# Kernel tuning notes

Hardware: AMD Instinct MI355X
Metric: run time of the kernel (lower is better)

Reference implementation:

```python
import jax, jax.numpy as jnp
import numpy as np

H = 512   # hidden_size
E = 512   # choice embedding dim (== hidden in the dummy init)
B = 256   # batch
T = 64    # arg sequence length
V = 10000 # number of choices


def setup_inputs() -> dict:
    key = jax.random.key(0)
    ks = jax.random.split(key, 10)
    s = 0.05
    return {
        "init_state": jax.random.normal(ks[0], (B, H), jnp.float32),
        "choice_embed": jax.random.normal(ks[1], (V, E), jnp.float32),
        "arg_seq": jax.random.randint(ks[2], (B, T), 0, V, jnp.int64),
        # flax LSTMCell equivalent: fused gate weights (order i, f, g, o)
        "Wx": jax.random.normal(ks[3], (E, 4 * H), jnp.float32) * s,
        "Wh": jax.random.normal(ks[4], (H, 4 * H), jnp.float32) * s,
        "b": jnp.zeros((4 * H,), jnp.float32),
        # MLP step-score head: concat(H, E) -> 256 -> 1
        "W1": jax.random.normal(ks[5], (H + E, 256), jnp.float32) * s,
        "b1": jnp.zeros((256,), jnp.float32),
        "W2": jax.random.normal(ks[6], (256, 1), jnp.float32) * s,
        "b2": jnp.zeros((1,), jnp.float32),
    }


def _forward(init_state, choice_embed, arg_seq, Wx, Wh, b, W1, b1, W2, b2):
    # initial carry: zeros + init_state, for both c and h
    c0 = init_state
    h0 = init_state
    x_seq = choice_embed[arg_seq]            # [B, T, E] embedding gather
    xs = jnp.swapaxes(x_seq, 0, 1)           # [T, B, E] for scan

    def step(carry, x):
        c, h = carry
        gates = x @ Wx + h @ Wh + b          # [B, 4H]
        i, f, g, o = jnp.split(gates, 4, axis=-1)
        i = jax.nn.sigmoid(i)
        f = jax.nn.sigmoid(f)
        g = jnp.tanh(g)
        o = jax.nn.sigmoid(o)
        c2 = f * c + i * g
        h2 = o * jnp.tanh(c2)
        return (c2, h2), h2

    _, hs = jax.lax.scan(step, (c0, h0), xs)  # hs: [T, B, H]
    hs = jnp.swapaxes(hs, 0, 1)               # [B, T, H]
    # state fed to the score head at step t is the hidden BEFORE consuming x_t
    state = jnp.concatenate((h0[:, None, :], hs[:, :-1, :]), axis=1)  # [B, T, H]
    state = state.reshape(-1, H)               # [B*T, H]

    feat = jnp.concatenate((state, x_seq.reshape(-1, E)), axis=-1)    # [B*T, H+E]
    hid = jax.nn.relu(feat @ W1 + b1)
    score = hid @ W2 + b2                      # [B*T, 1]
    step_scores = score.reshape(-1, T)         # [B, T]
    return jnp.sum(step_scores, axis=-1, keepdims=True)  # [B, 1]


def reference(init_state, choice_embed, arg_seq, Wx, Wh, b, W1, b1, W2, b2):
    return _forward(init_state, choice_embed, arg_seq, Wx, Wh, b, W1, b1, W2, b2)
```

## Files before the change

### kernel.cpp

```cpp
#include <hip/hip_runtime.h>
#include <hip/hip_bf16.h>
#include <math.h>

#define H   512
#define E   512
#define B_  256
#define T_  64
#define G4  2048
#define C1  256
#define BT  16384

#define SPIN_CAP (1 << 22)

typedef __attribute__((ext_vector_type(8))) short  short8;
typedef __attribute__((ext_vector_type(4))) float  f32x4;
typedef __attribute__((ext_vector_type(4))) int    i32x4;
typedef __attribute__((ext_vector_type(4))) unsigned short ushort4v;
typedef unsigned short ushort;
typedef unsigned long long u64;

#define PITCH_US 520

#define BAR_LGKM() asm volatile("s_waitcnt lgkmcnt(0)\n\ts_barrier" ::: "memory")
#define BAR_ALL()  asm volatile("s_waitcnt vmcnt(0) lgkmcnt(0)\n\ts_barrier" ::: "memory")

__device__ __forceinline__ ushort f2bf(float x) {
    unsigned u = __builtin_bit_cast(unsigned, x);
    unsigned r = (u + 0x7FFFu + ((u >> 16) & 1u)) >> 16;
    return (ushort)r;
}
__device__ __forceinline__ float fast_sig(float x) {
    return __builtin_amdgcn_rcpf(1.f + __expf(-x));
}
__device__ __forceinline__ float fast_tanh(float x) {
    return 1.f - 2.f * __builtin_amdgcn_rcpf(1.f + __expf(2.f * x));
}

#define LOAD4_SC0(v0,v1,v2,v3,p0,p1,p2,p3) \
  asm volatile("global_load_dwordx4 %0, %4, off sc0\n\t" \
               "global_load_dwordx4 %1, %5, off sc0\n\t" \
               "global_load_dwordx4 %2, %6, off sc0\n\t" \
               "global_load_dwordx4 %3, %7, off sc0\n\t" \
               "s_waitcnt vmcnt(0)" \
               : "=&v"(v0), "=&v"(v1), "=&v"(v2), "=&v"(v3) \
               : "v"(p0), "v"(p1), "v"(p2), "v"(p3) : "memory")
#define LOAD4_SC01(v0,v1,v2,v3,p0,p1,p2,p3) \
  asm volatile("global_load_dwordx4 %0, %4, off sc0 sc1\n\t" \
               "global_load_dwordx4 %1, %5, off sc0 sc1\n\t" \
               "global_load_dwordx4 %2, %6, off sc0 sc1\n\t" \
               "global_load_dwordx4 %3, %7, off sc0 sc1\n\t" \
               "s_waitcnt vmcnt(0)" \
               : "=&v"(v0), "=&v"(v1), "=&v"(v2), "=&v"(v3) \
               : "v"(p0), "v"(p1), "v"(p2), "v"(p3) : "memory")

__global__ __launch_bounds__(256) void prep_weights(
    const float* __restrict__ Wx, const float* __restrict__ Wh,
    const float* __restrict__ W1,
    ushort* __restrict__ WxT, ushort* __restrict__ WhT, ushort* __restrict__ W1T)
{
    __shared__ float t[32][33];
    int bx = blockIdx.x;
    const float* in; ushort* out; int K, N, k0, n0;
    if (bx < 1024)       { in = Wx; out = WxT; K = 512;  N = 2048; k0 = (bx >> 6) * 32; n0 = (bx & 63) * 32; }
    else if (bx < 2048)  { bx -= 1024; in = Wh; out = WhT; K = 512;  N = 2048; k0 = (bx >> 6) * 32; n0 = (bx & 63) * 32; }
    else                 { bx -= 2048; in = W1; out = W1T; K = 1024; N = 256;  k0 = (bx >> 3) * 32; n0 = (bx & 7) * 32; }
    const int tr = threadIdx.x >> 3;
    const int tc = (threadIdx.x & 7) * 4;
    float4 v = *(const float4*)(in + (size_t)(k0 + tr) * N + n0 + tc);
    t[tr][tc + 0] = v.x; t[tr][tc + 1] = v.y; t[tr][tc + 2] = v.z; t[tr][tc + 3] = v.w;
    __syncthreads();
    ushort4v o = { f2bf(t[tc + 0][tr]), f2bf(t[tc + 1][tr]),
                   f2bf(t[tc + 2][tr]), f2bf(t[tc + 3][tr]) };
    *(ushort4v*)(out + (size_t)(n0 + tr) * K + k0 + tc) = o;
}

__global__ __launch_bounds__(128) void gather_embed_bf16(
    const float* __restrict__ emb, const int* __restrict__ idx,
    ushort* __restrict__ X)
{
    const int r = blockIdx.x;
    const int v = idx[r];
    const int c = threadIdx.x * 4;
    float4 f = *(const float4*)(emb + (size_t)v * E + c);
    ushort4v o = { f2bf(f.x), f2bf(f.y), f2bf(f.z), f2bf(f.w) };
    *(ushort4v*)(X + (size_t)r * E + c) = o;
}

__global__ __launch_bounds__(128) void init_prep(
    const float* __restrict__ init, ushort* __restrict__ h0,
    ushort* __restrict__ S)
{
    const int r = blockIdx.x;
    const int c = threadIdx.x * 4;
    float4 f = *(const float4*)(init + (size_t)r * H + c);
    ushort4v o = { f2bf(f.x), f2bf(f.y), f2bf(f.z), f2bf(f.w) };
    *(ushort4v*)(h0 + (size_t)r * H + c) = o;
    *(ushort4v*)(S + ((size_t)r * T_) * H + c) = o;
}

__global__ __launch_bounds__(256) void zero_buf(int* p, int n) {
    int i = blockIdx.x * 256 + threadIdx.x;
    if (i < n) p[i] = 0;
}

__global__ __launch_bounds__(256, 1) void lstm_fused_main(
    const ushort* __restrict__ WhT, const ushort* __restrict__ WxT,
    const ushort* __restrict__ Xbf, const float* __restrict__ bg,
    const float*  __restrict__ init_state, const ushort* __restrict__ h0,
    ushort* __restrict__ pp0, ushort* __restrict__ pp1,
    ushort* __restrict__ S, int* __restrict__ xcd_tbl, int* __restrict__ cnts)
{
    __shared__ __align__(16) ushort hsh[16 * PITCH_US];
    __shared__ __align__(16) ushort xsh[2][16 * PITCH_US];
    __shared__ int exl[256];

    const int tid  = threadIdx.x;
    const int wave = tid >> 6, lane = tid & 63;
    const int quad = lane >> 4, l16 = lane & 15;

    int xcd;
    asm volatile("s_getreg_b32 %0, hwreg(HW_REG_XCC_ID)" : "=s"(xcd));
    if (tid == 0)
        __hip_atomic_store(&xcd_tbl[blockIdx.x], (xcd & 7) + 1,
                           __ATOMIC_RELAXED, __HIP_MEMORY_SCOPE_AGENT);
    if (wave == 0) {
        for (int it = 0; it < SPIN_CAP; ++it) {
            int miss = 0;
#pragma unroll
            for (int j = 0; j < 4; ++j) {
                int i = lane + j * 64;
                int v = __hip_atomic_load(&xcd_tbl[i], __ATOMIC_RELAXED,
                                          __HIP_MEMORY_SCOPE_AGENT);
                exl[i] = (v == 0) ? 0 : (v - 1);
                if (v == 0) miss = 1;
            }
            if (!__any(miss)) break;
            __builtin_amdgcn_s_sleep(4);
        }
    }
    BAR_LGKM();

    int g = 0, m = 0, loc = 0;
    {
        int cntx[8] = {0,0,0,0,0,0,0,0};
        for (int i = 0; i < 256; ++i) cntx[exl[i] & 7]++;
        int take[8], base[8], tA = 0;
        for (int x = 0; x < 8; ++x) {
            int tk = cntx[x] >> 4;
            if (tA + tk > 16) tk = 16 - tA;
            take[x] = tk; base[x] = tA; tA += tk;
        }
        int rc[8] = {0,0,0,0,0,0,0,0}, lc = 0;
        for (int i = 0; i < 256; ++i) {
            int x = exl[i] & 7, r = rc[x]++;
            if ((r >> 4) < take[x]) {
                if (i == (int)blockIdx.x) { g = base[x] + (r >> 4); m = r & 15; loc = 1; }
            } else {
                if (i == (int)blockIdx.x) { g = tA + (lc >> 4); m = lc & 15; loc = 0; }
                lc++;
            }
        }
    }

    const int n0   = g * 16;
    const int jw   = m * 32 + wave * 8;
    const int koff = quad * 8;
    const int ccol = jw + (quad & 1) * 4;
    const int myrow = n0 + l16;

    short8 af[2][16], ax[2][16];
#pragma unroll
    for (int mf = 0; mf < 2; ++mf) {
        const int gate = mf * 2 + (l16 >> 3);
        const size_t rowoff = (size_t)(gate * 512 + jw + (l16 & 7)) * 512 + koff;
        const ushort* bh = WhT + rowoff;
        const ushort* bx = WxT + rowoff;
#pragma unroll
        for (int kk = 0; kk < 16; ++kk) {
            af[mf][kk] = *(const short8*)(bh + kk * 32);
            ax[mf][kk] = *(const short8*)(bx + kk * 32);
        }
    }

    float bgi[4], bgf[4], bgg[4], bgo[4];
#pragma unroll
    for (int r = 0; r < 4; ++r) {
        bgi[r] = bg[ccol + r];
        bgf[r] = bg[512 + ccol + r];
        bgg[r] = bg[1024 + ccol + r];
        bgo[r] = bg[1536 + ccol + r];
    }

    float c[4];
    {
        const float* ip = init_state + (size_t)myrow * H + ccol;
#pragma unroll
        for (int r = 0; r < 4; ++r) c[r] = ip[r];
    }

    int gr[4], gc[4], lo[4];
#pragma unroll
    for (int j = 0; j < 4; ++j) {
        int lin = tid + j * 256;
        gr[j] = lin >> 6; gc[j] = lin & 63;
        lo[j] = gr[j] * PITCH_US + gc[j] * 8;
    }

#pragma unroll
    for (int j = 0; j < 4; ++j) {
        i32x4 v = *(const i32x4*)(Xbf + ((size_t)(n0 + gr[j]) * T_) * H + gc[j] * 8);
        *(i32x4*)&xsh[0][lo[j]] = v;
    }
    BAR_LGKM();

    int* cnt = cnts + g * 32;
    const int frag_base = l16 * PITCH_US + quad * 8;

    for (int t = 0; t < T_ - 1; ++t) {
        i32x4 xv0, xv1, xv2, xv3;
        const int have_x = (t + 1 < T_ - 1);
        if (have_x) {
            xv0 = *(const i32x4*)(Xbf + ((size_t)(n0 + gr[0]) * T_ + t + 1) * H + gc[0] * 8);
            xv1 = *(const i32x4*)(Xbf + ((size_t)(n0 + gr[1]) * T_ + t + 1) * H + gc[1] * 8);
            xv2 = *(const i32x4*)(Xbf + ((size_t)(n0 + gr[2]) * T_ + t + 1) * H + gc[2] * 8);
            xv3 = *(const i32x4*)(Xbf + ((size_t)(n0 + gr[3]) * T_ + t + 1) * H + gc[3] * 8);
        }

        f32x4 ax0 = {}, ax1 = {};
        {
            const ushort* xb = xsh[t & 1];
#pragma unroll
            for (int kk = 0; kk < 16; ++kk) {
                short8 b = *(const short8*)&xb[frag_base + kk * 32];
                ax0 = __builtin_amdgcn_mfma_f32_16x16x32_bf16(ax[0][kk], b, ax0, 0, 0, 0);
                ax1 = __builtin_amdgcn_mfma_f32_16x16x32_bf16(ax[1][kk], b, ax1, 0, 0, 0);
            }
        }

        if (t > 0) {
            const int tgt = t << 4;
            for (int it = 0; it < SPIN_CAP; ++it) {
                if (__hip_atomic_load(cnt, __ATOMIC_RELAXED,
                                      __HIP_MEMORY_SCOPE_AGENT) >= tgt) break;
                __builtin_amdgcn_s_sleep(1);
            }
        }

        {
            const ushort* hin = (t == 0) ? h0 : ((t & 1) ? pp0 : pp1);
            const ushort* p0 = hin + (size_t)(n0 + gr[0]) * H + gc[0] * 8;
            const ushort* p1 = hin + (size_t)(n0 + gr[1]) * H + gc[1] * 8;
            const ushort* p2 = hin + (size_t)(n0 + gr[2]) * H + gc[2] * 8;
            const ushort* p3 = hin + (size_t)(n0 + gr[3]) * H + gc[3] * 8;
            i32x4 v0, v1, v2, v3;
            if (loc) { LOAD4_SC0(v0, v1, v2, v3, p0, p1, p2, p3); }
            else     { LOAD4_SC01(v0, v1, v2, v3, p0, p1, p2, p3); }
            *(i32x4*)&hsh[lo[0]] = v0;
            *(i32x4*)&hsh[lo[1]] = v1;
            *(i32x4*)&hsh[lo[2]] = v2;
            *(i32x4*)&hsh[lo[3]] = v3;
        }
        BAR_LGKM();

        f32x4 a0 = {}, a1 = {};
#pragma unroll
        for (int kk = 0; kk < 16; ++kk) {
            short8 b = *(const short8*)&hsh[frag_base + kk * 32];
            a0 = __builtin_amdgcn_mfma_f32_16x16x32_bf16(af[0][kk], b, a0, 0, 0, 0);
            a1 = __builtin_amdgcn_mfma_f32_16x16x32_bf16(af[1][kk], b, a1, 0, 0, 0);
        }

        if (have_x) {
            ushort* xb = xsh[(t + 1) & 1];
            *(i32x4*)&xb[lo[0]] = xv0;
            *(i32x4*)&xb[lo[1]] = xv1;
            *(i32x4*)&xb[lo[2]] = xv2;
            *(i32x4*)&xb[lo[3]] = xv3;
        }

        float hv[4];
#pragma unroll
        for (int r = 0; r < 4; ++r) {
            float v0 = a0[r] + ax0[r], v1 = a1[r] + ax1[r];
            float p0 = __shfl_xor(v0, 32, 64);
            float p1 = __shfl_xor(v1, 32, 64);
            float iv = (quad < 2) ? v0 : p0;
            float fv = (quad < 2) ? p0 : v0;
            float gv = (quad < 2) ? v1 : p1;
            float ov = (quad < 2) ? p1 : v1;
            iv = fast_sig(iv + bgi[r]);
            fv = fast_sig(fv + bgf[r]);
            gv = fast_tanh(gv + bgg[r]);
            ov = fast_sig(ov + bgo[r]);
            float cn = fv * c[r] + iv * gv;
            c[r] = cn;
            hv[r] = ov * fast_tanh(cn);
        }

        ushort4v o4 = { f2bf(hv[0]), f2bf(hv[1]), f2bf(hv[2]), f2bf(hv[3]) };
        ushort* hout = (t & 1) ? pp1 : pp0;
        if (quad < 2) {
            u64* hp = (u64*)(hout + (size_t)myrow * H + ccol);
            if (loc) *hp = __builtin_bit_cast(u64, o4);
            else __hip_atomic_store(hp, __builtin_bit_cast(u64, o4),
                                    __ATOMIC_RELAXED, __HIP_MEMORY_SCOPE_AGENT);
        }

        BAR_ALL();
        if (tid == 0) atomicAdd(cnt, 1);

        if (quad < 2)
            *(ushort4v*)(S + ((size_t)myrow * T_ + (t + 1)) * H + ccol) = o4;
    }
}

__global__ __launch_bounds__(256) void gemm_score(
    const ushort* __restrict__ Sm, const ushort* __restrict__ Xbf,
    const ushort* __restrict__ W1T,
    const float* __restrict__ b1, const float* __restrict__ W2,
    float* __restrict__ scores)
{
    const int tid  = threadIdx.x;
    const int wave = tid >> 6, lane = tid & 63;
    const int quad = lane >> 4, l16 = lane & 15;
    const int m0 = blockIdx.y * 128 + wave * 32;
    const int n0 = blockIdx.x * 64;
    const int koff = quad * 8;

    f32x4 acc[2][4] = {};

    for (int src = 0; src < 2; ++src) {
        const ushort* A  = src ? Xbf : Sm;
        const ushort* Bm = W1T + src * 512;
        const ushort* a0p = A + (size_t)(m0 + l16) * H + koff;
        const ushort* a1p = A + (size_t)(m0 + 16 + l16) * H + koff;
        const ushort* bp  = Bm + (size_t)(n0 + l16) * 1024 + koff;
        for (int kk = 0; kk < H; kk += 32) {
            short8 a0 = *(const short8*)(a0p + kk);
            short8 a1 = *(const short8*)(a1p + kk);
#pragma unroll
            for (int nf = 0; nf < 4; ++nf) {
                short8 b = *(const short8*)(bp + (size_t)nf * 16 * 1024 + kk);
                acc[0][nf] = __builtin_amdgcn_mfma_f32_16x16x32_bf16(a0, b, acc[0][nf], 0, 0, 0);
                acc[1][nf] = __builtin_amdgcn_mfma_f32_16x16x32_bf16(a1, b, acc[1][nf], 0, 0, 0);
            }
        }
    }

    float w2v[4], b1v[4];
#pragma unroll
    for (int nf = 0; nf < 4; ++nf) {
        const int col = n0 + nf * 16 + l16;
        w2v[nf] = W2[col];
        b1v[nf] = b1[col];
    }

#pragma unroll
    for (int mf = 0; mf < 2; ++mf) {
#pragma unroll
        for (int r = 0; r < 4; ++r) {
            float p = 0.f;
#pragma unroll
            for (int nf = 0; nf < 4; ++nf)
                p += fmaxf(acc[mf][nf][r] + b1v[nf], 0.f) * w2v[nf];
            p += __shfl_xor(p, 1, 64);
            p += __shfl_xor(p, 2, 64);
            p += __shfl_xor(p, 4, 64);
            p += __shfl_xor(p, 8, 64);
            if (l16 == 0)
                atomicAdd(&scores[m0 + mf * 16 + quad * 4 + r], p);
        }
    }
}

__global__ __launch_bounds__(64) void reduce_scores(
    const float* __restrict__ scores, const float* __restrict__ b2,
    float* __restrict__ out)
{
    const int b    = blockIdx.x;
    const int lane = threadIdx.x;
    float s = scores[(size_t)b * T_ + lane] + b2[0];
#pragma unroll
    for (int off = 32; off; off >>= 1) s += __shfl_xor(s, off, 64);
    if (lane == 0) out[b] = s;
}

extern "C" void kernel_launch(void* const* d_in, const int* in_sizes, int n_in,
                              void* d_out, int out_size, void* d_ws, size_t ws_size,
                              hipStream_t stream)
{
    const float* init_state = (const float*)d_in[0];
    const float* choice_emb = (const float*)d_in[1];
    const int*   arg_seq    = (const int*)  d_in[2];
    const float* Wx         = (const float*)d_in[3];
    const float* Wh         = (const float*)d_in[4];
    const float* bg         = (const float*)d_in[5];
    const float* W1         = (const float*)d_in[6];
    const float* b1         = (const float*)d_in[7];
    const float* W2         = (const float*)d_in[8];
    const float* b2         = (const float*)d_in[9];
    float* out = (float*)d_out;

    ushort* WxT = (ushort*)d_ws;
    ushort* WhT = WxT + 1048576;
    ushort* W1T = WhT + 1048576;
    ushort* Xbf = W1T + 262144;
    ushort* S   = Xbf + 8388608;
    ushort* h0  = S   + 8388608;
    ushort* pp0 = h0  + 131072;
    ushort* pp1 = pp0 + 131072;
    float*  scores  = (float*)(pp1 + 131072);
    int*    xcd_tbl = (int*)(scores + BT);
    int*    cnts    = xcd_tbl + 256;

    zero_buf<<<70, 256, 0, stream>>>((int*)scores, BT + 256 + 512);

    prep_weights<<<2304, 256, 0, stream>>>(Wx, Wh, W1, WxT, WhT, W1T);

    gather_embed_bf16<<<BT, 128, 0, stream>>>(choice_emb, arg_seq, Xbf);
    init_prep<<<B_, 128, 0, stream>>>(init_state, h0, S);

    lstm_fused_main<<<256, 256, 0, stream>>>(
        WhT, WxT, Xbf, bg, init_state, h0, pp0, pp1, S, xcd_tbl, cnts);

    gemm_score<<<dim3(C1 / 64, BT / 128), 256, 0, stream>>>(
        S, Xbf, W1T, b1, W2, scores);
    reduce_scores<<<B_, 64, 0, stream>>>(scores, b2, out);
}
```

Baseline: 383.8 us.

## Replace block barrier and shared atomic counter with per-wave flags and direct loads

The recurrent LSTM kernel no longer stages h and x through shared memory behind block-wide barriers. Each wave loads its B-operand fragments straight from global memory into registers. Each wave also publishes its own progress flag instead of a single atomicAdd counter per group, and waiters poll all flags with a wave-wide vote. This removes the s_barrier and shared-memory round trips on the critical serial path. In exchange it adds more global load traffic (fragments are reloaded per wave rather than shared), loses the x prefetch overlap, and introduces a capped poll loop.

Measured after the change: 701.2 us. 82.7% more time.

```diff
diff --git a/kernel.cpp b/kernel.cpp
--- a/kernel.cpp
+++ b/kernel.cpp
@@ -11,18 +11,16 @@
 #define BT  16384
 
 #define SPIN_CAP (1 << 22)
+#define POLL_CAP (1 << 18)
 
 typedef __attribute__((ext_vector_type(8))) short  short8;
 typedef __attribute__((ext_vector_type(4))) float  f32x4;
-typedef __attribute__((ext_vector_type(4))) int    i32x4;
 typedef __attribute__((ext_vector_type(4))) unsigned short ushort4v;
 typedef unsigned short ushort;
 typedef unsigned long long u64;
 
-#define PITCH_US 520
 
 #define BAR_LGKM() asm volatile("s_waitcnt lgkmcnt(0)\n\ts_barrier" ::: "memory")
-#define BAR_ALL()  asm volatile("s_waitcnt vmcnt(0) lgkmcnt(0)\n\ts_barrier" ::: "memory")
 
 __device__ __forceinline__ ushort f2bf(float x) {
     unsigned u = __builtin_bit_cast(unsigned, x);
@@ -36,22 +34,13 @@
     return 1.f - 2.f * __builtin_amdgcn_rcpf(1.f + __expf(2.f * x));
 }
 
-#define LOAD4_SC0(v0,v1,v2,v3,p0,p1,p2,p3) \
-  asm volatile("global_load_dwordx4 %0, %4, off sc0\n\t" \
-               "global_load_dwordx4 %1, %5, off sc0\n\t" \
-               "global_load_dwordx4 %2, %6, off sc0\n\t" \
-               "global_load_dwordx4 %3, %7, off sc0\n\t" \
-               "s_waitcnt vmcnt(0)" \
-               : "=&v"(v0), "=&v"(v1), "=&v"(v2), "=&v"(v3) \
-               : "v"(p0), "v"(p1), "v"(p2), "v"(p3) : "memory")
-#define LOAD4_SC01(v0,v1,v2,v3,p0,p1,p2,p3) \
-  asm volatile("global_load_dwordx4 %0, %4, off sc0 sc1\n\t" \
-               "global_load_dwordx4 %1, %5, off sc0 sc1\n\t" \
-               "global_load_dwordx4 %2, %6, off sc0 sc1\n\t" \
-               "global_load_dwordx4 %3, %7, off sc0 sc1\n\t" \
-               "s_waitcnt vmcnt(0)" \
-               : "=&v"(v0), "=&v"(v1), "=&v"(v2), "=&v"(v3) \
-               : "v"(p0), "v"(p1), "v"(p2), "v"(p3) : "memory")
+#define HLOAD4(SC, b0,b1,b2,b3, base, O0,O1,O2,O3) \
+  asm volatile("global_load_dwordx4 %0, %4, off offset:" #O0 " " #SC "\n\t" \
+               "global_load_dwordx4 %1, %4, off offset:" #O1 " " #SC "\n\t" \
+               "global_load_dwordx4 %2, %4, off offset:" #O2 " " #SC "\n\t" \
+               "global_load_dwordx4 %3, %4, off offset:" #O3 " " #SC \
+               : "=&v"(b0), "=&v"(b1), "=&v"(b2), "=&v"(b3) \
+               : "v"(base) : "memory")
 
 __global__ __launch_bounds__(256) void prep_weights(
     const float* __restrict__ Wx, const float* __restrict__ Wh,
@@ -110,8 +99,6 @@
     ushort* __restrict__ pp0, ushort* __restrict__ pp1,
     ushort* __restrict__ S, int* __restrict__ xcd_tbl, int* __restrict__ cnts)
 {
-    __shared__ __align__(16) ushort hsh[16 * PITCH_US];
-    __shared__ __align__(16) ushort xsh[2][16 * PITCH_US];
     __shared__ int exl[256];
 
     const int tid  = threadIdx.x;
@@ -198,84 +185,55 @@
         for (int r = 0; r < 4; ++r) c[r] = ip[r];
     }
 
-    int gr[4], gc[4], lo[4];
-#pragma unroll
-    for (int j = 0; j < 4; ++j) {
-        int lin = tid + j * 256;
-        gr[j] = lin >> 6; gc[j] = lin & 63;
-        lo[j] = gr[j] * PITCH_US + gc[j] * 8;
-    }
-
-#pragma unroll
-    for (int j = 0; j < 4; ++j) {
-        i32x4 v = *(const i32x4*)(Xbf + ((size_t)(n0 + gr[j]) * T_) * H + gc[j] * 8);
-        *(i32x4*)&xsh[0][lo[j]] = v;
-    }
-    BAR_LGKM();
-
-    int* cnt = cnts + g * 32;
-    const int frag_base = l16 * PITCH_US + quad * 8;
+    int* slots = cnts + g * 64;
+    int* myslotp = slots + m * 4 + wave;
+    const int* pollp = slots + lane;
+
+    const ushort* xbase = Xbf + ((size_t)myrow * T_) * H + koff;
 
     for (int t = 0; t < T_ - 1; ++t) {
-        i32x4 xv0, xv1, xv2, xv3;
-        const int have_x = (t + 1 < T_ - 1);
-        if (have_x) {
-            xv0 = *(const i32x4*)(Xbf + ((size_t)(n0 + gr[0]) * T_ + t + 1) * H + gc[0] * 8);
-            xv1 = *(const i32x4*)(Xbf + ((size_t)(n0 + gr[1]) * T_ + t + 1) * H + gc[1] * 8);
-            xv2 = *(const i32x4*)(Xbf + ((size_t)(n0 + gr[2]) * T_ + t + 1) * H + gc[2] * 8);
-            xv3 = *(const i32x4*)(Xbf + ((size_t)(n0 + gr[3]) * T_ + t + 1) * H + gc[3] * 8);
-        }
-
+        const ushort* xp = xbase + (size_t)t * H;
+        short8 bx[16];
+#pragma unroll
+        for (int kk = 0; kk < 16; ++kk) bx[kk] = *(const short8*)(xp + kk * 32);
         f32x4 ax0 = {}, ax1 = {};
-        {
-            const ushort* xb = xsh[t & 1];
-#pragma unroll
-            for (int kk = 0; kk < 16; ++kk) {
-                short8 b = *(const short8*)&xb[frag_base + kk * 32];
-                ax0 = __builtin_amdgcn_mfma_f32_16x16x32_bf16(ax[0][kk], b, ax0, 0, 0, 0);
-                ax1 = __builtin_amdgcn_mfma_f32_16x16x32_bf16(ax[1][kk], b, ax1, 0, 0, 0);
-            }
+#pragma unroll
+        for (int kk = 0; kk < 16; ++kk) {
+            ax0 = __builtin_amdgcn_mfma_f32_16x16x32_bf16(ax[0][kk], bx[kk], ax0, 0, 0, 0);
+            ax1 = __builtin_amdgcn_mfma_f32_16x16x32_bf16(ax[1][kk], bx[kk], ax1, 0, 0, 0);
         }
 
         if (t > 0) {
-            const int tgt = t << 4;
-            for (int it = 0; it < SPIN_CAP; ++it) {
-                if (__hip_atomic_load(cnt, __ATOMIC_RELAXED,
-                                      __HIP_MEMORY_SCOPE_AGENT) >= tgt) break;
+            for (int it = 0; it < POLL_CAP; ++it) {
+                int v = __hip_atomic_load(pollp, __ATOMIC_RELAXED,
+                                          __HIP_MEMORY_SCOPE_AGENT);
+                if (__all(v >= t)) break;
                 __builtin_amdgcn_s_sleep(1);
             }
         }
 
-        {
-            const ushort* hin = (t == 0) ? h0 : ((t & 1) ? pp0 : pp1);
-            const ushort* p0 = hin + (size_t)(n0 + gr[0]) * H + gc[0] * 8;
-            const ushort* p1 = hin + (size_t)(n0 + gr[1]) * H + gc[1] * 8;
-            const ushort* p2 = hin + (size_t)(n0 + gr[2]) * H + gc[2] * 8;
-            const ushort* p3 = hin + (size_t)(n0 + gr[3]) * H + gc[3] * 8;
-            i32x4 v0, v1, v2, v3;
-            if (loc) { LOAD4_SC0(v0, v1, v2, v3, p0, p1, p2, p3); }
-            else     { LOAD4_SC01(v0, v1, v2, v3, p0, p1, p2, p3); }
-            *(i32x4*)&hsh[lo[0]] = v0;
-            *(i32x4*)&hsh[lo[1]] = v1;
-            *(i32x4*)&hsh[lo[2]] = v2;
-            *(i32x4*)&hsh[lo[3]] = v3;
-        }
-        BAR_LGKM();
+        const ushort* hin = (t == 0) ? h0 : ((t & 1) ? pp0 : pp1);
+        const ushort* hp = hin + (size_t)myrow * H + koff;
+        short8 bh[16];
+        if (loc) {
+            HLOAD4(sc0, bh[0], bh[1], bh[2], bh[3],  hp,   0,  64, 128, 192);
+            HLOAD4(sc0, bh[4], bh[5], bh[6], bh[7],  hp, 256, 320, 384, 448);
+            HLOAD4(sc0, bh[8], bh[9], bh[10],bh[11], hp, 512, 576, 640, 704);
+            HLOAD4(sc0, bh[12],bh[13],bh[14],bh[15], hp, 768, 832, 896, 960);
+        } else {
+            HLOAD4(sc0 sc1, bh[0], bh[1], bh[2], bh[3],  hp,   0,  64, 128, 192);
+            HLOAD4(sc0 sc1, bh[4], bh[5], bh[6], bh[7],  hp, 256, 320, 384, 448);
+            HLOAD4(sc0 sc1, bh[8], bh[9], bh[10],bh[11], hp, 512, 576, 640, 704);
+            HLOAD4(sc0 sc1, bh[12],bh[13],bh[14],bh[15], hp, 768, 832, 896, 960);
+        }
+        asm volatile("s_waitcnt vmcnt(0)" ::: "memory");
+        __builtin_amdgcn_sched_barrier(0);
 
         f32x4 a0 = {}, a1 = {};
 #pragma unroll
         for (int kk = 0; kk < 16; ++kk) {
-            short8 b = *(const short8*)&hsh[frag_base + kk * 32];
-            a0 = __builtin_amdgcn_mfma_f32_16x16x32_bf16(af[0][kk], b, a0, 0, 0, 0);
-            a1 = __builtin_amdgcn_mfma_f32_16x16x32_bf16(af[1][kk], b, a1, 0, 0, 0);
-        }
-
-        if (have_x) {
-            ushort* xb = xsh[(t + 1) & 1];
-            *(i32x4*)&xb[lo[0]] = xv0;
-            *(i32x4*)&xb[lo[1]] = xv1;
-            *(i32x4*)&xb[lo[2]] = xv2;
-            *(i32x4*)&xb[lo[3]] = xv3;
+            a0 = __builtin_amdgcn_mfma_f32_16x16x32_bf16(af[0][kk], bh[kk], a0, 0, 0, 0);
+            a1 = __builtin_amdgcn_mfma_f32_16x16x32_bf16(af[1][kk], bh[kk], a1, 0, 0, 0);
         }
 
         float hv[4];
@@ -300,14 +258,16 @@
         ushort4v o4 = { f2bf(hv[0]), f2bf(hv[1]), f2bf(hv[2]), f2bf(hv[3]) };
         ushort* hout = (t & 1) ? pp1 : pp0;
         if (quad < 2) {
-            u64* hp = (u64*)(hout + (size_t)myrow * H + ccol);
-            if (loc) *hp = __builtin_bit_cast(u64, o4);
-            else __hip_atomic_store(hp, __builtin_bit_cast(u64, o4),
+            u64* hp2 = (u64*)(hout + (size_t)myrow * H + ccol);
+            if (loc) *hp2 = __builtin_bit_cast(u64, o4);
+            else __hip_atomic_store(hp2, __builtin_bit_cast(u64, o4),
                                     __ATOMIC_RELAXED, __HIP_MEMORY_SCOPE_AGENT);
         }
 
-        BAR_ALL();
-        if (tid == 0) atomicAdd(cnt, 1);
+        asm volatile("s_waitcnt vmcnt(0)" ::: "memory");
+        if (lane == 0)
+            __hip_atomic_store(myslotp, t + 1, __ATOMIC_RELAXED,
+                               __HIP_MEMORY_SCOPE_AGENT);
 
         if (quad < 2)
             *(ushort4v*)(S + ((size_t)myrow * T_ + (t + 1)) * H + ccol) = o4;
@@ -413,7 +373,7 @@
     int*    xcd_tbl = (int*)(scores + BT);
     int*    cnts    = xcd_tbl + 256;
 
-    zero_buf<<<70, 256, 0, stream>>>((int*)scores, BT + 256 + 512);
+    zero_buf<<<72, 256, 0, stream>>>((int*)scores, BT + 256 + 1024);
 
     prep_weights<<<2304, 256, 0, stream>>>(Wx, Wh, W1, WxT, WhT, W1T);
 
```

## Use 8 waves per block in LSTM recurrence with one MFMA chain per wave

Applied to the files above, without the earlier changes.

Doubles the LSTM recurrence block to 512 threads. Each wave now owns 4 hidden columns and runs a single MFMA accumulation chain instead of two, which halves the serial MFMA latency per step. Gate values are redistributed with three cross-quad shuffles so that each lane computes one hidden unit. The h tile is loaded cooperatively by twice as many threads, and the spin cap is lowered. In exchange there are more waves per barrier, scalar 2-byte h and S stores that replace 8-byte vector stores, and more shuffle work.

Measured after the change: 377.8 us. About the same (-1.6%).

```diff
diff --git a/kernel.cpp b/kernel.cpp
--- a/kernel.cpp
+++ b/kernel.cpp
@@ -11,6 +11,7 @@
 #define BT  16384
 
 #define SPIN_CAP (1 << 22)
+#define POLL_CAP (1 << 18)
 
 typedef __attribute__((ext_vector_type(8))) short  short8;
 typedef __attribute__((ext_vector_type(4))) float  f32x4;
@@ -24,6 +25,7 @@
 #define BAR_LGKM() asm volatile("s_waitcnt lgkmcnt(0)\n\ts_barrier" ::: "memory")
 #define BAR_ALL()  asm volatile("s_waitcnt vmcnt(0) lgkmcnt(0)\n\ts_barrier" ::: "memory")
 
+
 __device__ __forceinline__ ushort f2bf(float x) {
     unsigned u = __builtin_bit_cast(unsigned, x);
     unsigned r = (u + 0x7FFFu + ((u >> 16) & 1u)) >> 16;
@@ -36,22 +38,16 @@
     return 1.f - 2.f * __builtin_amdgcn_rcpf(1.f + __expf(2.f * x));
 }
 
-#define LOAD4_SC0(v0,v1,v2,v3,p0,p1,p2,p3) \
-  asm volatile("global_load_dwordx4 %0, %4, off sc0\n\t" \
-               "global_load_dwordx4 %1, %5, off sc0\n\t" \
-               "global_load_dwordx4 %2, %6, off sc0\n\t" \
-               "global_load_dwordx4 %3, %7, off sc0\n\t" \
+#define LOAD2_SC0(v0,v1,p0,p1) \
+  asm volatile("global_load_dwordx4 %0, %2, off sc0\n\t" \
+               "global_load_dwordx4 %1, %3, off sc0\n\t" \
                "s_waitcnt vmcnt(0)" \
-               : "=&v"(v0), "=&v"(v1), "=&v"(v2), "=&v"(v3) \
-               : "v"(p0), "v"(p1), "v"(p2), "v"(p3) : "memory")
-#define LOAD4_SC01(v0,v1,v2,v3,p0,p1,p2,p3) \
-  asm volatile("global_load_dwordx4 %0, %4, off sc0 sc1\n\t" \
-               "global_load_dwordx4 %1, %5, off sc0 sc1\n\t" \
-               "global_load_dwordx4 %2, %6, off sc0 sc1\n\t" \
-               "global_load_dwordx4 %3, %7, off sc0 sc1\n\t" \
+               : "=&v"(v0), "=&v"(v1) : "v"(p0), "v"(p1) : "memory")
+#define LOAD2_SC01(v0,v1,p0,p1) \
+  asm volatile("global_load_dwordx4 %0, %2, off sc0 sc1\n\t" \
+               "global_load_dwordx4 %1, %3, off sc0 sc1\n\t" \
                "s_waitcnt vmcnt(0)" \
-               : "=&v"(v0), "=&v"(v1), "=&v"(v2), "=&v"(v3) \
-               : "v"(p0), "v"(p1), "v"(p2), "v"(p3) : "memory")
+               : "=&v"(v0), "=&v"(v1) : "v"(p0), "v"(p1) : "memory")
 
 __global__ __launch_bounds__(256) void prep_weights(
     const float* __restrict__ Wx, const float* __restrict__ Wh,
@@ -103,7 +99,7 @@
     if (i < n) p[i] = 0;
 }
 
-__global__ __launch_bounds__(256, 1) void lstm_fused_main(
+__global__ __launch_bounds__(512, 2) void lstm_fused_main(
     const ushort* __restrict__ WhT, const ushort* __restrict__ WxT,
     const ushort* __restrict__ Xbf, const float* __restrict__ bg,
     const float*  __restrict__ init_state, const ushort* __restrict__ h0,
@@ -162,52 +158,41 @@
         }
     }
 
-    const int n0   = g * 16;
-    const int jw   = m * 32 + wave * 8;
-    const int koff = quad * 8;
-    const int ccol = jw + (quad & 1) * 4;
+    const int n0    = g * 16;
+    const int jw    = m * 32 + wave * 4;
+    const int koff  = quad * 8;
     const int myrow = n0 + l16;
-
-    short8 af[2][16], ax[2][16];
-#pragma unroll
-    for (int mf = 0; mf < 2; ++mf) {
-        const int gate = mf * 2 + (l16 >> 3);
-        const size_t rowoff = (size_t)(gate * 512 + jw + (l16 & 7)) * 512 + koff;
+    const int hcol  = jw + quad;
+
+    short8 af[16], ax[16];
+    {
+        const size_t rowoff =
+            (size_t)((l16 >> 2) * 512 + jw + (l16 & 3)) * 512 + koff;
         const ushort* bh = WhT + rowoff;
         const ushort* bx = WxT + rowoff;
 #pragma unroll
         for (int kk = 0; kk < 16; ++kk) {
-            af[mf][kk] = *(const short8*)(bh + kk * 32);
-            ax[mf][kk] = *(const short8*)(bx + kk * 32);
-        }
-    }
-
-    float bgi[4], bgf[4], bgg[4], bgo[4];
-#pragma unroll
-    for (int r = 0; r < 4; ++r) {
-        bgi[r] = bg[ccol + r];
-        bgf[r] = bg[512 + ccol + r];
-        bgg[r] = bg[1024 + ccol + r];
-        bgo[r] = bg[1536 + ccol + r];
-    }
-
-    float c[4];
-    {
-        const float* ip = init_state + (size_t)myrow * H + ccol;
-#pragma unroll
-        for (int r = 0; r < 4; ++r) c[r] = ip[r];
-    }
-
-    int gr[4], gc[4], lo[4];
-#pragma unroll
-    for (int j = 0; j < 4; ++j) {
-        int lin = tid + j * 256;
+            af[kk] = *(const short8*)(bh + kk * 32);
+            ax[kk] = *(const short8*)(bx + kk * 32);
+        }
+    }
+
+    float bgq[4];
+#pragma unroll
+    for (int r = 0; r < 4; ++r) bgq[r] = bg[quad * 512 + jw + r];
+
+    float c1 = init_state[(size_t)myrow * H + hcol];
+
+    int gr[2], gc[2], lo[2];
+#pragma unroll
+    for (int j = 0; j < 2; ++j) {
+        int lin = tid + j * 512;
         gr[j] = lin >> 6; gc[j] = lin & 63;
         lo[j] = gr[j] * PITCH_US + gc[j] * 8;
     }
 
 #pragma unroll
-    for (int j = 0; j < 4; ++j) {
+    for (int j = 0; j < 2; ++j) {
         i32x4 v = *(const i32x4*)(Xbf + ((size_t)(n0 + gr[j]) * T_) * H + gc[j] * 8);
         *(i32x4*)&xsh[0][lo[j]] = v;
     }
@@ -217,29 +202,26 @@
     const int frag_base = l16 * PITCH_US + quad * 8;
 
     for (int t = 0; t < T_ - 1; ++t) {
-        i32x4 xv0, xv1, xv2, xv3;
+        i32x4 xv0, xv1;
         const int have_x = (t + 1 < T_ - 1);
         if (have_x) {
             xv0 = *(const i32x4*)(Xbf + ((size_t)(n0 + gr[0]) * T_ + t + 1) * H + gc[0] * 8);
             xv1 = *(const i32x4*)(Xbf + ((size_t)(n0 + gr[1]) * T_ + t + 1) * H + gc[1] * 8);
-            xv2 = *(const i32x4*)(Xbf + ((size_t)(n0 + gr[2]) * T_ + t + 1) * H + gc[2] * 8);
-            xv3 = *(const i32x4*)(Xbf + ((size_t)(n0 + gr[3]) * T_ + t + 1) * H + gc[3] * 8);
-        }
-
-        f32x4 ax0 = {}, ax1 = {};
+        }
+
+        f32x4 axx = {};
         {
             const ushort* xb = xsh[t & 1];
 #pragma unroll
             for (int kk = 0; kk < 16; ++kk) {
                 short8 b = *(const short8*)&xb[frag_base + kk * 32];
-                ax0 = __builtin_amdgcn_mfma_f32_16x16x32_bf16(ax[0][kk], b, ax0, 0, 0, 0);
-                ax1 = __builtin_amdgcn_mfma_f32_16x16x32_bf16(ax[1][kk], b, ax1, 0, 0, 0);
+                axx = __builtin_amdgcn_mfma_f32_16x16x32_bf16(ax[kk], b, axx, 0, 0, 0);
             }
         }
 
         if (t > 0) {
             const int tgt = t << 4;
-            for (int it = 0; it < SPIN_CAP; ++it) {
+            for (int it = 0; it < POLL_CAP; ++it) {
                 if (__hip_atomic_load(cnt, __ATOMIC_RELAXED,
                                       __HIP_MEMORY_SCOPE_AGENT) >= tgt) break;
                 __builtin_amdgcn_s_sleep(1);
@@ -250,67 +232,65 @@
             const ushort* hin = (t == 0) ? h0 : ((t & 1) ? pp0 : pp1);
             const ushort* p0 = hin + (size_t)(n0 + gr[0]) * H + gc[0] * 8;
             const ushort* p1 = hin + (size_t)(n0 + gr[1]) * H + gc[1] * 8;
-            const ushort* p2 = hin + (size_t)(n0 + gr[2]) * H + gc[2] * 8;
-            const ushort* p3 = hin + (size_t)(n0 + gr[3]) * H + gc[3] * 8;
-            i32x4 v0, v1, v2, v3;
-            if (loc) { LOAD4_SC0(v0, v1, v2, v3, p0, p1, p2, p3); }
-            else     { LOAD4_SC01(v0, v1, v2, v3, p0, p1, p2, p3); }
+            i32x4 v0, v1;
+            if (loc) { LOAD2_SC0(v0, v1, p0, p1); }
+            else     { LOAD2_SC01(v0, v1, p0, p1); }
             *(i32x4*)&hsh[lo[0]] = v0;
             *(i32x4*)&hsh[lo[1]] = v1;
-            *(i32x4*)&hsh[lo[2]] = v2;
-            *(i32x4*)&hsh[lo[3]] = v3;
         }
         BAR_LGKM();
 
-        f32x4 a0 = {}, a1 = {};
+        f32x4 ah = {};
 #pragma unroll
         for (int kk = 0; kk < 16; ++kk) {
             short8 b = *(const short8*)&hsh[frag_base + kk * 32];
-            a0 = __builtin_amdgcn_mfma_f32_16x16x32_bf16(af[0][kk], b, a0, 0, 0, 0);
-            a1 = __builtin_amdgcn_mfma_f32_16x16x32_bf16(af[1][kk], b, a1, 0, 0, 0);
+            ah = __builtin_amdgcn_mfma_f32_16x16x32_bf16(af[kk], b, ah, 0, 0, 0);
         }
 
         if (have_x) {
             ushort* xb = xsh[(t + 1) & 1];
             *(i32x4*)&xb[lo[0]] = xv0;
             *(i32x4*)&xb[lo[1]] = xv1;
-            *(i32x4*)&xb[lo[2]] = xv2;
-            *(i32x4*)&xb[lo[3]] = xv3;
-        }
-
-        float hv[4];
-#pragma unroll
-        for (int r = 0; r < 4; ++r) {
-            float v0 = a0[r] + ax0[r], v1 = a1[r] + ax1[r];
-            float p0 = __shfl_xor(v0, 32, 64);
-            float p1 = __shfl_xor(v1, 32, 64);
-            float iv = (quad < 2) ? v0 : p0;
-            float fv = (quad < 2) ? p0 : v0;
-            float gv = (quad < 2) ? v1 : p1;
-            float ov = (quad < 2) ? p1 : v1;
-            iv = fast_sig(iv + bgi[r]);
-            fv = fast_sig(fv + bgf[r]);
-            gv = fast_tanh(gv + bgg[r]);
-            ov = fast_sig(ov + bgo[r]);
-            float cn = fv * c[r] + iv * gv;
-            c[r] = cn;
-            hv[r] = ov * fast_tanh(cn);
-        }
-
-        ushort4v o4 = { f2bf(hv[0]), f2bf(hv[1]), f2bf(hv[2]), f2bf(hv[3]) };
+        }
+
+        float g4[4];
+#pragma unroll
+        for (int r = 0; r < 4; ++r) g4[r] = ah[r] + axx[r] + bgq[r];
+        float s1 = (quad & 1) ? ((quad & 2) ? g4[2] : g4[0])
+                              : ((quad & 2) ? g4[3] : g4[1]);
+        float s2 = (quad & 2) ? ((quad & 1) ? g4[1] : g4[0])
+                              : ((quad & 1) ? g4[3] : g4[2]);
+        float s3 = (quad & 2) ? ((quad & 1) ? g4[0] : g4[1])
+                              : ((quad & 1) ? g4[2] : g4[3]);
+        float r0 = (quad & 1) ? ((quad & 2) ? g4[3] : g4[1])
+                              : ((quad & 2) ? g4[2] : g4[0]);
+        float r1 = __shfl_xor(s1, 16, 64);
+        float r2 = __shfl_xor(s2, 32, 64);
+        float r3 = __shfl_xor(s3, 48, 64);
+        float iv = (quad == 0) ? r0 : (quad == 1) ? r1 : (quad == 2) ? r2 : r3;
+        float fv = (quad == 0) ? r1 : (quad == 1) ? r0 : (quad == 2) ? r3 : r2;
+        float gv = (quad == 0) ? r2 : (quad == 1) ? r3 : (quad == 2) ? r0 : r1;
+        float ov = (quad == 0) ? r3 : (quad == 1) ? r2 : (quad == 2) ? r1 : r0;
+        iv = fast_sig(iv);
+        fv = fast_sig(fv);
+        gv = fast_tanh(gv);
+        ov = fast_sig(ov);
+        float cn = fv * c1 + iv * gv;
+        c1 = cn;
+        ushort ho = f2bf(ov * fast_tanh(cn));
+
         ushort* hout = (t & 1) ? pp1 : pp0;
-        if (quad < 2) {
-            u64* hp = (u64*)(hout + (size_t)myrow * H + ccol);
-            if (loc) *hp = __builtin_bit_cast(u64, o4);
-            else __hip_atomic_store(hp, __builtin_bit_cast(u64, o4),
-                                    __ATOMIC_RELAXED, __HIP_MEMORY_SCOPE_AGENT);
+        {
+            ushort* hp2 = hout + (size_t)myrow * H + hcol;
+            if (loc) *hp2 = ho;
+            else asm volatile("global_store_short %0, %1, off sc0 sc1"
+                              :: "v"(hp2), "v"((int)ho) : "memory");
         }
 
         BAR_ALL();
         if (tid == 0) atomicAdd(cnt, 1);
 
-        if (quad < 2)
-            *(ushort4v*)(S + ((size_t)myrow * T_ + (t + 1)) * H + ccol) = o4;
+        S[((size_t)myrow * T_ + (t + 1)) * H + hcol] = ho;
     }
 }
 
@@ -420,7 +400,7 @@
     gather_embed_bf16<<<BT, 128, 0, stream>>>(choice_emb, arg_seq, Xbf);
     init_prep<<<B_, 128, 0, stream>>>(init_state, h0, S);
 
-    lstm_fused_main<<<256, 256, 0, stream>>>(
+    lstm_fused_main<<<256, 512, 0, stream>>>(
         WhT, WxT, Xbf, bg, init_state, h0, pp0, pp1, S, xcd_tbl, cnts);
 
     gemm_score<<<dim3(C1 / 64, BT / 128), 256, 0, stream>>>(
```
